# Optimization experiments

Hardware: AMD Instinct MI355X
Metric: run time of the kernel (lower is better)

## Reference

```python
import jax, jax.numpy as jnp
import numpy as np

B, NPG, K, C, IN_DIM, GS_DIM, NBLK, NCLF = 8, 12500, 128, 128, 7, 11, 4, 5
N = B * NPG          # 100000 total nodes
E = N * 8            # 800000 nnz in block-diagonal complex gradient operator


def setup_inputs() -> dict:
    key = jax.random.key(0)
    ks = jax.random.split(key, 20)
    x = jax.random.normal(ks[0], (N, IN_DIM), jnp.float32)
    evals = jax.random.uniform(ks[1], (B, K), jnp.float32) * 10.0  # nonneg eigenvalues
    evecs = jax.random.normal(ks[2], (N, K), jnp.float32) / np.float32(np.sqrt(NPG))
    mass = jax.random.uniform(ks[3], (N,), jnp.float32) + 0.1      # positive lumped mass
    graph_stats = jax.random.normal(ks[4], (B, GS_DIM), jnp.float32)
    batch = jnp.repeat(jnp.arange(B, dtype=jnp.int32), NPG)        # sorted graph ids
    epg = E // B
    offs = jnp.repeat(jnp.arange(B, dtype=jnp.int32) * NPG, epg)   # block-diagonal structure
    grad_rows = jax.random.randint(ks[5], (E,), 0, NPG, jnp.int32) + offs
    grad_cols = jax.random.randint(ks[6], (E,), 0, NPG, jnp.int32) + offs
    grad_vals_re = jax.random.normal(ks[7], (E,), jnp.float32) * 0.1
    grad_vals_im = jax.random.normal(ks[8], (E,), jnp.float32) * 0.1
    grad_n = jnp.full((B,), NPG, jnp.int32)
    s = lambda k, sh, fan: jax.random.normal(k, sh, jnp.float32) / np.float32(np.sqrt(fan))
    W_embed = s(ks[9], (IN_DIM, C), IN_DIM); b_embed = jnp.zeros((C,), jnp.float32)
    t_diff = jax.random.uniform(ks[10], (NBLK, C), jnp.float32) * 0.5 + 1e-3
    A_grad = s(ks[11], (NBLK, C, C), C)
    W1 = s(ks[12], (NBLK, 3 * C, C), 3 * C); b1 = jnp.zeros((NBLK, C), jnp.float32)
    W2 = s(ks[13], (NBLK, C, C), C);         b2 = jnp.zeros((NBLK, C), jnp.float32)
    Wh1 = s(ks[14], (C + GS_DIM, 64), C + GS_DIM); bh1 = jnp.zeros((64,), jnp.float32)
    Wh2 = s(ks[15], (64, NCLF), 64);               bh2 = jnp.zeros((NCLF,), jnp.float32)
    return dict(x=x, evals=evals, evecs=evecs, mass=mass, graph_stats=graph_stats,
                batch=batch, grad_rows=grad_rows, grad_cols=grad_cols,
                grad_vals_re=grad_vals_re, grad_vals_im=grad_vals_im, grad_n=grad_n,
                W_embed=W_embed, b_embed=b_embed, t_diff=t_diff, A_grad=A_grad,
                W1=W1, b1=b1, W2=W2, b2=b2, Wh1=Wh1, bh1=bh1, Wh2=Wh2, bh2=bh2)


def _forward(x, evals, evecs, mass, graph_stats, batch, grad_rows, grad_cols,
             vre, vim, W_embed, b_embed, t_diff, A_grad, W1, b1, W2, b2,
             Wh1, bh1, Wh2, bh2):
    n = x.shape[0]
    ev_r = evecs.reshape(B, NPG, K)              # per-graph spectral basis (equal-size graphs)
    h = jax.nn.relu(x @ W_embed + b_embed)       # embed: [N, C]
    for blk in range(NBLK):                      # fixed small number of blocks
        # --- learned-time spectral diffusion ---
        time = jnp.clip(jnp.abs(t_diff[blk]), 1e-8)            # [C]
        hm = (h * mass[:, None]).reshape(B, NPG, C)
        spec = jnp.einsum('bnk,bnc->bkc', ev_r, hm)            # to_basis: [B, K, C]
        spec = spec * jnp.exp(-evals[:, :, None] * time[None, None, :])
        h_diff = jnp.einsum('bnk,bkc->bnc', ev_r, spec).reshape(n, C)
        # --- block-sparse complex gradient: g = (vre + i*vim) @ h_diff ---
        xg = h_diff[grad_cols]                                 # [E, C] gather
        g_re = jnp.zeros((n, C), h.dtype).at[grad_rows].add(vre[:, None] * xg)
        g_im = jnp.zeros((n, C), h.dtype).at[grad_rows].add(vim[:, None] * xg)
        # --- spatial gradient features: tanh(Re(conj(g) * (A g))) ---
        A = A_grad[blk]
        g_feat = jnp.tanh(g_re * (g_re @ A.T) + g_im * (g_im @ A.T))
        # --- per-vertex MLP + residual (dropout = eval-mode identity) ---
        comb = jnp.concatenate([h, h_diff, g_feat], axis=-1)   # [N, 3C]
        h = h + (jax.nn.relu(comb @ W1[blk] + b1[blk]) @ W2[blk] + b2[blk])
    # --- fuse per-node features with gathered graph stats, node clf head ---
    fused = jnp.concatenate([h, graph_stats[batch]], axis=-1)  # [N, C+11]
    return jax.nn.relu(fused @ Wh1 + bh1) @ Wh2 + bh2          # [N, 5]


def reference(x, evals, evecs, mass, graph_stats, batch, grad_rows, grad_cols,
              grad_vals_re, grad_vals_im, grad_n, W_embed, b_embed, t_diff,
              A_grad, W1, b1, W2, b2, Wh1, bh1, Wh2, bh2):
    # Vectorized replacement of the original per-batch .item() nnz-count loop
    # (histogram of edge rows into per-graph node-offset bins); the block-sparse
    # operator is applied directly with global COO indices so nnz is only a stat.
    node_off = jnp.concatenate([jnp.zeros((1,), jnp.int32),
                                jnp.cumsum(grad_n)[:-1].astype(jnp.int32)])
    _grad_nnz = jnp.bincount(jnp.searchsorted(node_off, grad_rows, side='right') - 1, length=B)
    return _forward(x, evals, evecs, mass, graph_stats, batch, grad_rows, grad_cols,
                    grad_vals_re, grad_vals_im, W_embed, b_embed, t_diff, A_grad,
                    W1, b1, W2, b2, Wh1, bh1, Wh2, bh2)
```

## Files before the change

### kernel.cpp

```cpp
#include <hip/hip_runtime.h>
#include <hip/hip_bf16.h>

#define NNODES 100000
#define NPG    12500
#define NGRAPH 8
#define KD     128
#define CD     128
#define INDIM  7
#define GSDIM  11
#define NBLKS  4
#define NCLF   5
#define NEDGE  800000
#define BCAP   32
#define NPGP   12800
#define TBSPLIT 40
#define TBCHUNK 320
#define NTILES  196
#define NT32    391
#define NT128   98

typedef __attribute__((ext_vector_type(8))) short short8v;
typedef __attribute__((ext_vector_type(4))) float f32x4;
typedef unsigned short u16;
typedef unsigned long long u64;

#define MFMA(acc, a, b) acc = __builtin_amdgcn_mfma_f32_16x16x32_bf16(a, b, acc, 0, 0, 0)

__device__ __forceinline__ u16 f2b(float f) {
  union { __hip_bfloat16 h; u16 u; } cv;
  cv.h = __float2bfloat16(f);
  return cv.u;
}
__device__ __forceinline__ float b2f(u16 u) {
  return __uint_as_float((unsigned)u << 16);
}


__device__ __forceinline__ void stage64_f32(u16* S, const float* src, int ld, int k0, int valid) {
  int t = threadIdx.x, row = t >> 2, kq = t & 3;
  alignas(16) u16 tmp[8] = {0, 0, 0, 0, 0, 0, 0, 0};
  if (row < valid) {
    const float* p = src + (size_t)row * ld + k0 + kq * 8;
    float4 f0 = *(const float4*)p, f1 = *(const float4*)(p + 4);
    tmp[0] = f2b(f0.x); tmp[1] = f2b(f0.y); tmp[2] = f2b(f0.z); tmp[3] = f2b(f0.w);
    tmp[4] = f2b(f1.x); tmp[5] = f2b(f1.y); tmp[6] = f2b(f1.z); tmp[7] = f2b(f1.w);
  }
  *(uint4*)&S[row * 40 + kq * 8] = *(uint4*)tmp;
}

__device__ __forceinline__ void stage64_b16(u16* S, const u16* src, long ld, int k0, int valid) {
  int t = threadIdx.x, row = t >> 2, kq = t & 3;
  uint4 v = make_uint4(0, 0, 0, 0);
  if (row < valid) v = *(const uint4*)(src + (size_t)row * ld + k0 + kq * 8);
  *(uint4*)&S[row * 40 + kq * 8] = v;
}

__device__ __forceinline__ void stage32_b16(u16* S, const u16* src, long ld, int k0, int valid) {
  int t = threadIdx.x;
  if (t < 128) {
    int row = t >> 2, kq = t & 3;
    uint4 v = make_uint4(0, 0, 0, 0);
    if (row < valid) v = *(const uint4*)(src + (size_t)row * ld + k0 + kq * 8);
    *(uint4*)&S[row * 40 + kq * 8] = v;
  }
}

__device__ __forceinline__ void stB512(u16* S, const u16* src, int k0) {
  int t = threadIdx.x, row = t >> 2, kq = t & 3;
  uint4 v = *(const uint4*)(src + (size_t)row * 128 + k0 + kq * 8);
  *(uint4*)&S[row * 40 + kq * 8] = v;
}

__device__ __forceinline__ void stage128_b16(u16* S, const u16* src, long ld, int k0) {
  int t = threadIdx.x, row = t >> 1, half = t & 1;
  const u16* p = src + (size_t)row * ld + k0 + half * 16;
  uint4 v0 = *(const uint4*)p, v1 = *(const uint4*)(p + 8);
  *(uint4*)&S[row * 40 + half * 16] = v0;
  *(uint4*)&S[row * 40 + half * 16 + 8] = v1;
}

__device__ __forceinline__ void stage128_f32(u16* S, const float* src, int ld, int k0) {
  int t = threadIdx.x, row = t >> 1, half = t & 1;
  const float* p = src + (size_t)row * ld + k0 + half * 16;
  float4 f0 = *(const float4*)p, f1 = *(const float4*)(p + 4);
  float4 f2 = *(const float4*)(p + 8), f3 = *(const float4*)(p + 12);
  alignas(16) u16 tmp[16];
  tmp[0] = f2b(f0.x); tmp[1] = f2b(f0.y); tmp[2]  = f2b(f0.z); tmp[3]  = f2b(f0.w);
  tmp[4] = f2b(f1.x); tmp[5] = f2b(f1.y); tmp[6]  = f2b(f1.z); tmp[7]  = f2b(f1.w);
  tmp[8] = f2b(f2.x); tmp[9] = f2b(f2.y); tmp[10] = f2b(f2.z); tmp[11] = f2b(f2.w);
  tmp[12] = f2b(f3.x); tmp[13] = f2b(f3.y); tmp[14] = f2b(f3.z); tmp[15] = f2b(f3.w);
  *(uint4*)&S[row * 40 + half * 16] = *(uint4*)&tmp[0];
  *(uint4*)&S[row * 40 + half * 16 + 8] = *(uint4*)&tmp[8];
}

__device__ __forceinline__ short8v frag(const u16* S, int row0, int l) {
  return *(const short8v*)&S[(row0 + (l & 15)) * 40 + (l >> 4) * 8];
}
__device__ __forceinline__ short8v frag_p(const u16* S, int row0, int l, int pitch, int k0) {
  return *(const short8v*)&S[(row0 + (l & 15)) * pitch + k0 + (l >> 4) * 8];
}


__global__ void k_fill0(float4* p, int n4) {
  int i = blockIdx.x * blockDim.x + threadIdx.x;
  int s = gridDim.x * blockDim.x;
  float4 z = make_float4(0.f, 0.f, 0.f, 0.f);
  for (; i < n4; i += s) p[i] = z;
}

__global__ __launch_bounds__(256) void k_embed2(const float* __restrict__ x,
                                                const float* __restrict__ W,
                                                const float* __restrict__ bv,
                                                const float* __restrict__ mass,
                                                u16* __restrict__ h16,
                                                u16* __restrict__ hmT) {
  int b = blockIdx.x / 200, tile = blockIdx.x % 200;
  int n0 = tile * 64;
  size_t gbase = (size_t)b * NPG;
  int t = threadIdx.x;
  __shared__ float xs[64][8];
  __shared__ float Ws[INDIM][128];
  __shared__ float bs[128];
  __shared__ float ms[64];
  __shared__ float ld[64][132];
  if (t < 128) bs[t] = bv[t];
  for (int i = t; i < INDIM * 128; i += 256) Ws[i >> 7][i & 127] = W[i];
  for (int i = t; i < 64 * INDIM; i += 256) {
    int r = i / INDIM, q = i % INDIM;
    int gn = n0 + r;
    xs[r][q] = (gn < NPG) ? x[(gbase + gn) * INDIM + q] : 0.f;
  }
  if (t < 64) {
    int gn = n0 + t;
    ms[t] = (gn < NPG) ? mass[gbase + gn] : 0.f;
  }
  __syncthreads();
  {
    int row = t & 63, c0 = (t >> 6) * 32;
#pragma unroll
    for (int cc = 0; cc < 32; ++cc) {
      int c = c0 + cc;
      float acc = bs[c];
#pragma unroll
      for (int i = 0; i < INDIM; ++i) acc = fmaf(xs[row][i], Ws[i][c], acc);
      ld[row][c] = fmaxf(acc, 0.f);
    }
  }
  __syncthreads();
  {
    int row = t >> 2, q = t & 3;
    if (n0 + row < NPG) {
      size_t base = (gbase + n0 + row) * (size_t)CD + q * 32;
      alignas(16) u16 tmp[8];
#pragma unroll
      for (int u = 0; u < 4; ++u) {
#pragma unroll
        for (int i = 0; i < 8; ++i) tmp[i] = f2b(ld[row][q * 32 + u * 8 + i]);
        *(uint4*)&h16[base + u * 8] = *(uint4*)tmp;
      }
    }
  }
  {
    int crow = t >> 1, half = t & 1;
    alignas(16) u16 tmp[8];
#pragma unroll
    for (int q = 0; q < 4; ++q) {
      int nb = half * 32 + q * 8;
#pragma unroll
      for (int i = 0; i < 8; ++i) tmp[i] = f2b(ld[nb + i][crow] * ms[nb + i]);
      *(uint4*)&hmT[((size_t)(b * 128 + crow)) * NPGP + n0 + nb] = *(uint4*)tmp;
    }
  }
}

__global__ void k_bucket_place(const int* __restrict__ rows, const int* __restrict__ cols,
                               const float* __restrict__ vre, const float* __restrict__ vim,
                               int* cnt, u64* bucket) {
  int e = blockIdx.x * 256 + threadIdx.x;
  if (e >= NEDGE) return;
  int r = rows[e];
  int pos = atomicAdd(&cnt[r], 1);
  if (pos < BCAP) {
    u64 ent = (u64)(unsigned)cols[e]
            | ((u64)f2b(vre[e]) << 32)
            | ((u64)f2b(vim[e]) << 48);
    bucket[(size_t)r * BCAP + pos] = ent;
  }
}

__global__ void k_gather_ev(const int* __restrict__ cnt, const u64* __restrict__ bucket,
                            const float* __restrict__ evf, const u16* __restrict__ ev16,
                            int useB16,
                            u16* __restrict__ gre, u16* __restrict__ gim) {
  int orig = blockIdx.x;
  int blk  = (orig & 7) * 3125 + (orig >> 3);
  int wv = threadIdx.x >> 6;
  int ln = threadIdx.x & 63;
  int r  = blk * 4 + wv;
  int d = min(cnt[r], BCAP);
  const u64* bk = bucket + (size_t)r * BCAP;
  float2 ra0 = make_float2(0.f, 0.f), ia0 = make_float2(0.f, 0.f);
  float2 ra1 = make_float2(0.f, 0.f), ia1 = make_float2(0.f, 0.f);
  if (useB16) {
    int i = 0;
    for (; i + 2 <= d; i += 2) {
      u64 e0 = bk[i], e1 = bk[i + 1];
      int c0 = (int)(unsigned)e0, c1 = (int)(unsigned)e1;
      float a0 = b2f((u16)(e0 >> 32)), b0 = b2f((u16)(e0 >> 48));
      float a1 = b2f((u16)(e1 >> 32)), b1 = b2f((u16)(e1 >> 48));
      ushort2 u0 = *(const ushort2*)&ev16[(size_t)c0 * KD + ln * 2];
      ushort2 u1 = *(const ushort2*)&ev16[(size_t)c1 * KD + ln * 2];
      float vx0 = b2f(u0.x), vy0 = b2f(u0.y);
      float vx1 = b2f(u1.x), vy1 = b2f(u1.y);
      ra0.x = fmaf(a0, vx0, ra0.x); ra0.y = fmaf(a0, vy0, ra0.y);
      ia0.x = fmaf(b0, vx0, ia0.x); ia0.y = fmaf(b0, vy0, ia0.y);
      ra1.x = fmaf(a1, vx1, ra1.x); ra1.y = fmaf(a1, vy1, ra1.y);
      ia1.x = fmaf(b1, vx1, ia1.x); ia1.y = fmaf(b1, vy1, ia1.y);
    }
    if (i < d) {
      u64 e0 = bk[i];
      int c0 = (int)(unsigned)e0;
      float a0 = b2f((u16)(e0 >> 32)), b0 = b2f((u16)(e0 >> 48));
      ushort2 u0 = *(const ushort2*)&ev16[(size_t)c0 * KD + ln * 2];
      float vx0 = b2f(u0.x), vy0 = b2f(u0.y);
      ra0.x = fmaf(a0, vx0, ra0.x); ra0.y = fmaf(a0, vy0, ra0.y);
      ia0.x = fmaf(b0, vx0, ia0.x); ia0.y = fmaf(b0, vy0, ia0.y);
    }
  } else {
    for (int i = 0; i < d; ++i) {
      u64 e0 = bk[i];
      int c0 = (int)(unsigned)e0;
      float a = b2f((u16)(e0 >> 32)), b = b2f((u16)(e0 >> 48));
      float2 v = *(const float2*)&evf[(size_t)c0 * KD + ln * 2];
      ra0.x = fmaf(a, v.x, ra0.x); ra0.y = fmaf(a, v.y, ra0.y);
      ia0.x = fmaf(b, v.x, ia0.x); ia0.y = fmaf(b, v.y, ia0.y);
    }
  }
  ushort2 ro, io;
  ro.x = f2b(ra0.x + ra1.x); ro.y = f2b(ra0.y + ra1.y);
  io.x = f2b(ia0.x + ia1.x); io.y = f2b(ia0.y + ia1.y);
  *(ushort2*)&gre[(size_t)r * KD + ln * 2] = ro;
  *(ushort2*)&gim[(size_t)r * KD + ln * 2] = io;
}

__global__ void k_prep_w(const float* __restrict__ W1, const float* __restrict__ W2,
                         u16* W1aT, u16* W1bT, u16* W1cT, u16* W2T) {
  int idx = blockIdx.x * 256 + threadIdx.x;
  int blk = idx >> 16, rem = idx & 65535;
  int mat = rem >> 14, e = rem & 16383;
  int j = e >> 7, c = e & 127;
  float v;
  u16* dst;
  if (mat < 3) {
    v = W1[(size_t)blk * 3 * 16384 + (size_t)mat * 16384 + e];
    dst = (mat == 0) ? W1aT : (mat == 1 ? W1bT : W1cT);
  } else {
    v = W2[(size_t)blk * 16384 + e];
    dst = W2T;
  }
  dst[(size_t)blk * 16384 + c * 128 + j] = f2b(v);
}

__global__ void k_prep_head(const float* __restrict__ Wh1, const float* __restrict__ Wh2,
                            u16* __restrict__ B1T, u16* __restrict__ B2T) {
  for (int idx = threadIdx.x; idx < 64 * 160; idx += 256) {
    int c = idx / 160, k = idx % 160;
    B1T[idx] = f2b(k < (CD + GSDIM) ? Wh1[k * 64 + c] : 0.f);
  }
  for (int idx = threadIdx.x; idx < 16 * 64; idx += 256) {
    int c = idx >> 6, k = idx & 63;
    B2T[idx] = f2b(c < NCLF ? Wh2[k * NCLF + c] : 0.f);
  }
}

__global__ void k_transpose_nk(const float* __restrict__ src, u16* __restrict__ dst,
                               u16* __restrict__ ev16, int writeMir) {
  int b = blockIdx.x / 200, tile = blockIdx.x % 200;
  int n0 = tile * 64;
  size_t gbase = (size_t)b * NPG;
  int t = threadIdx.x;
  __shared__ float ld[64][132];
  int row0 = t >> 5, c4 = t & 31;
#pragma unroll
  for (int it = 0; it < 8; ++it) {
    int r = it * 8 + row0;
    int gn = n0 + r;
    float4 v = make_float4(0.f, 0.f, 0.f, 0.f);
    if (gn < NPG) v = *(const float4*)&src[(gbase + gn) * KD + c4 * 4];
    *(float4*)&ld[r][c4 * 4] = v;
    if (writeMir && gn < NPG) {
      ushort4 o;
      o.x = f2b(v.x); o.y = f2b(v.y); o.z = f2b(v.z); o.w = f2b(v.w);
      *(ushort4*)&ev16[(gbase + gn) * KD + c4 * 4] = o;
    }
  }
  __syncthreads();
  int crow = t >> 1, half = t & 1;
  alignas(16) u16 tmp[8];
#pragma unroll
  for (int q = 0; q < 4; ++q) {
    int nb = half * 32 + q * 8;
#pragma unroll
    for (int i = 0; i < 8; ++i) tmp[i] = f2b(ld[nb + i][crow]);
    *(uint4*)&dst[((size_t)(b * 128 + crow)) * NPGP + n0 + nb] = *(uint4*)tmp;
  }
}


__global__ __launch_bounds__(256) void k_tobasis(const u16* __restrict__ evT,
                                                 const u16* __restrict__ hmT,
                                                 float* __restrict__ partials) {
  int g = blockIdx.x;
  int kt = g & 1;
  int s  = (g >> 1) % TBSPLIT;
  int b  = g / (2 * TBSPLIT);
  int t = threadIdx.x, w = t >> 6, l = t & 63;
  __shared__ u16 As[64 * 40];
  __shared__ u16 Bs[128 * 40];
  f32x4 acc[8];
  f32x4 z = {0.f, 0.f, 0.f, 0.f};
#pragma unroll
  for (int j = 0; j < 8; ++j) acc[j] = z;
  const u16* ae = evT + ((size_t)(b * 128 + kt * 64)) * NPGP + s * TBCHUNK;
  const u16* bh = hmT + (size_t)b * 128 * NPGP + s * TBCHUNK;
  for (int ks = 0; ks < TBCHUNK / 32; ++ks) {
    stage64_b16(As, ae, NPGP, ks * 32, 64);
    stage128_b16(Bs, bh, NPGP, ks * 32);
    __syncthreads();
    short8v a = frag(As, w * 16, l);
    __builtin_amdgcn_s_setprio(1);
#pragma unroll
    for (int j = 0; j < 8; ++j) MFMA(acc[j], a, frag(Bs, j * 16, l));
    __builtin_amdgcn_s_setprio(0);
    __syncthreads();
  }
  float* op = partials + (size_t)(b * TBSPLIT + s) * 16384 + kt * 64 * 128;
#pragma unroll
  for (int j = 0; j < 8; ++j)
#pragma unroll
    for (int i = 0; i < 4; ++i) {
      int krow = w * 16 + (l >> 4) * 4 + i;
      int c = j * 16 + (l & 15);
      op[krow * 128 + c] = acc[j][i];
    }
}

__global__ void k_reduce_scale_t(const float* __restrict__ partials,
                                 const float* __restrict__ evals,
                                 const float* __restrict__ td,
                                 float* __restrict__ spec, u16* __restrict__ specT) {
  int b = blockIdx.x >> 6;
  int idx = (blockIdx.x & 63) * 256 + threadIdx.x;
  int k = idx >> 7, c = idx & 127;
  float s = 0.f;
#pragma unroll 8
  for (int sp = 0; sp < TBSPLIT; ++sp)
    s += partials[(size_t)(b * TBSPLIT + sp) * 16384 + idx];
  float tm = fmaxf(fabsf(td[c]), 1e-8f);
  s *= expf(-evals[b * KD + k] * tm);
  spec[(size_t)b * 16384 + idx] = s;
  specT[(size_t)b * 16384 + c * 128 + k] = f2b(s);
}

__global__ __launch_bounds__(256) void k_smallT(const float* __restrict__ Agrad_blk,
                                                const u16* __restrict__ W1bT_blk,
                                                const float* __restrict__ spec,
                                                u16* __restrict__ SAT, u16* __restrict__ M1T) {
  int b = blockIdx.x & 7;
  int job = (blockIdx.x >> 3) & 1;
  int q = blockIdx.x >> 4;
  int t = threadIdx.x, w = t >> 6, l = t & 63;
  __shared__ u16 As[128 * 40];
  __shared__ u16 Bs[128 * 40];
  f32x4 acc[2][2];
  f32x4 z = {0.f, 0.f, 0.f, 0.f};
#pragma unroll
  for (int mi = 0; mi < 2; ++mi) { acc[mi][0] = z; acc[mi][1] = z; }
  for (int ks = 0; ks < 4; ++ks) {
    if (job == 0) stage128_f32(As, Agrad_blk, 128, ks * 32);
    else          stage128_b16(As, W1bT_blk, 128, ks * 32);
    stage128_f32(Bs, spec + (size_t)b * 16384, 128, ks * 32);
    __syncthreads();
    short8v a0 = frag(As, q * 32, l);
    short8v a1 = frag(As, q * 32 + 16, l);
#pragma unroll
    for (int jj = 0; jj < 2; ++jj) {
      short8v bj = frag(Bs, (w * 2 + jj) * 16, l);
      MFMA(acc[0][jj], a0, bj);
      MFMA(acc[1][jj], a1, bj);
    }
    __syncthreads();
  }
  u16* out = (job == 0 ? SAT : M1T) + (size_t)b * 16384;
#pragma unroll
  for (int mi = 0; mi < 2; ++mi)
#pragma unroll
    for (int jj = 0; jj < 2; ++jj)
#pragma unroll
      for (int i = 0; i < 4; ++i)
        out[(q * 32 + mi * 16 + (l >> 4) * 4 + i) * 128 + (w * 2 + jj) * 16 + (l & 15)] =
            f2b(acc[mi][jj][i]);
}

__global__ __launch_bounds__(256) void k_gfeat(const u16* __restrict__ Gre,
                                               const u16* __restrict__ Gim,
                                               const u16* __restrict__ specT,
                                               const u16* __restrict__ SAT,
                                               u16* __restrict__ gf) {
  int b = blockIdx.x / NT32, tile = blockIdx.x % NT32;
  int n0 = tile * 32;
  size_t gbase = (size_t)b * NPG;
  int t = threadIdx.x, w = t >> 6, l = t & 63;
  int r0 = (w & 1) * 16, c0 = (w >> 1) * 64;
  __shared__ u16 Sr[32 * 40];
  __shared__ u16 Si[32 * 40];
  __shared__ u16 Bs[128 * 40];
  __shared__ u16 Ba[128 * 40];
  f32x4 aGR[4], aAR[4], aGI[4], aAI[4];
  f32x4 z = {0.f, 0.f, 0.f, 0.f};
#pragma unroll
  for (int j = 0; j < 4; ++j) { aGR[j] = z; aAR[j] = z; aGI[j] = z; aAI[j] = z; }
  int valid = min(32, NPG - n0);
  const u16* gre = Gre + (gbase + n0) * KD;
  const u16* gim = Gim + (gbase + n0) * KD;
  for (int ks = 0; ks < 4; ++ks) {
    stage32_b16(Sr, gre, KD, ks * 32, valid);
    stage32_b16(Si, gim, KD, ks * 32, valid);
    stage128_b16(Bs, specT + (size_t)b * 16384, 128, ks * 32);
    stage128_b16(Ba, SAT + (size_t)b * 16384, 128, ks * 32);
    __syncthreads();
    short8v fr = frag(Sr, r0, l);
    short8v fi = frag(Si, r0, l);
    __builtin_amdgcn_s_setprio(1);
#pragma unroll
    for (int j = 0; j < 4; ++j) {
      short8v bs = frag(Bs, c0 + j * 16, l);
      short8v ba = frag(Ba, c0 + j * 16, l);
      MFMA(aGR[j], fr, bs);
      MFMA(aAR[j], fr, ba);
      MFMA(aGI[j], fi, bs);
      MFMA(aAI[j], fi, ba);
    }
    __builtin_amdgcn_s_setprio(0);
    __syncthreads();
  }
#pragma unroll
  for (int j = 0; j < 4; ++j) {
    int c = c0 + j * 16 + (l & 15);
#pragma unroll
    for (int i = 0; i < 4; ++i) {
      int n = n0 + r0 + (l >> 4) * 4 + i;
      if (n - n0 < valid) {
        float v = tanhf(fmaf(aGR[j][i], aAR[j][i], aGI[j][i] * aAI[j][i]));
        gf[(gbase + n) * CD + c] = f2b(v);
      }
    }
  }
}

__global__ __launch_bounds__(512) void k_mlp12(const float* __restrict__ evf,
                                               const u16* __restrict__ ev16,
                                               int useB16,
                                               const u16* __restrict__ gf,
                                               const u16* __restrict__ W1aT,
                                               const u16* __restrict__ M1T,
                                               const u16* __restrict__ W1cT,
                                               const float* __restrict__ b1,
                                               const u16* __restrict__ W2T,
                                               const float* __restrict__ b2,
                                               const float* __restrict__ mass,
                                               u16* __restrict__ h16,
                                               u16* __restrict__ hmT,
                                               int writeHmT) {
  int b = blockIdx.x / NT128, tile = blockIdx.x % NT128;
  int n0 = tile * 128;
  size_t gbase = (size_t)b * NPG;
  int t = threadIdx.x, w = t >> 6, l = t & 63;
  __shared__ u16 SH[27136];
  u16* As  = SH;
  u16* Bs  = SH + 5120;
  u16* t1S = SH + 10240;
  u16* Tm  = SH;
  f32x4 acc[8];
  f32x4 z = {0.f, 0.f, 0.f, 0.f};
#pragma unroll
  for (int j = 0; j < 8; ++j) acc[j] = z;
  int valid = min(128, NPG - n0);
  int r0 = w * 16;

  for (int seg = 0; seg < 3; ++seg) {
    const u16* bt = (seg == 0) ? W1aT : (seg == 1 ? M1T + (size_t)b * 16384 : W1cT);
    for (int ks = 0; ks < 4; ++ks) {
      if (seg == 0)      stage64_b16(As, h16 + (gbase + n0) * CD, CD, ks * 32, valid);
      else if (seg == 1) {
        if (useB16) stage64_b16(As, ev16 + (gbase + n0) * KD, KD, ks * 32, valid);
        else        stage64_f32(As, evf + (gbase + n0) * KD, KD, ks * 32, valid);
      }
      else               stage64_b16(As, gf + (gbase + n0) * CD, CD, ks * 32, valid);
      stB512(Bs, bt, ks * 32);
      __syncthreads();
      short8v a = frag(As, r0, l);
      __builtin_amdgcn_s_setprio(1);
#pragma unroll
      for (int j = 0; j < 8; ++j) MFMA(acc[j], a, frag(Bs, j * 16, l));
      __builtin_amdgcn_s_setprio(0);
      __syncthreads();
    }
  }
#pragma unroll
  for (int j = 0; j < 8; ++j) {
    int c = j * 16 + (l & 15);
    float bias = b1[c];
#pragma unroll
    for (int i = 0; i < 4; ++i) {
      int row = r0 + (l >> 4) * 4 + i;
      t1S[row * 132 + c] = f2b(fmaxf(acc[j][i] + bias, 0.f));
    }
  }
  __syncthreads();

#pragma unroll
  for (int j = 0; j < 8; ++j) acc[j] = z;
  for (int ks = 0; ks < 4; ++ks) {
    stB512(Bs, W2T, ks * 32);
    __syncthreads();
    short8v a = frag_p(t1S, r0, l, 132, ks * 32);
    __builtin_amdgcn_s_setprio(1);
#pragma unroll
    for (int j = 0; j < 8; ++j) MFMA(acc[j], a, frag(Bs, j * 16, l));
    __builtin_amdgcn_s_setprio(0);
    __syncthreads();
  }

  float massv[4];
#pragma unroll
  for (int i = 0; i < 4; ++i) {
    int nl = r0 + (l >> 4) * 4 + i;
    massv[i] = (nl < valid) ? mass[gbase + n0 + nl] : 0.f;
  }
#pragma unroll
  for (int j = 0; j < 8; ++j) {
    int c = j * 16 + (l & 15);
    float bias = b2[c];
#pragma unroll
    for (int i = 0; i < 4; ++i) {
      int nl = r0 + (l >> 4) * 4 + i;
      float hv = 0.f;
      if (nl < valid) {
        size_t idx = (gbase + n0 + nl) * (size_t)CD + c;
        hv = b2f(h16[idx]) + acc[j][i] + bias;
        h16[idx] = f2b(hv);
      }
      if (writeHmT) Tm[c * 130 + nl] = f2b(hv * massv[i]);
    }
  }
  if (writeHmT) {
    __syncthreads();
#pragma unroll
    for (int q = 0; q < 4; ++q) {
      int lin = t + q * 512;
      int cc = lin >> 4, chunk = lin & 15;
      *(uint4*)&hmT[((size_t)(b * 128 + cc)) * NPGP + n0 + chunk * 8] =
          *(const uint4*)&Tm[cc * 130 + chunk * 8];
    }
  }
}

__global__ __launch_bounds__(256) void k_head2(
    const u16* __restrict__ h16, const float* __restrict__ gs,
    const int* __restrict__ batch, const u16* __restrict__ B1T,
    const float* __restrict__ bh1, const u16* __restrict__ B2T,
    const float* __restrict__ bh2, float* __restrict__ out) {
  int n0 = blockIdx.x * 64;
  int t = threadIdx.x, w = t >> 6, l = t & 63;
  __shared__ u16 As[64 * 40];
  __shared__ u16 Bs[64 * 40];
  __shared__ u16 zS[64 * 72];
  int valid = min(64, NNODES - n0);
  f32x4 acc1[4];
  f32x4 z = {0.f, 0.f, 0.f, 0.f};
#pragma unroll
  for (int j = 0; j < 4; ++j) acc1[j] = z;
  for (int ks = 0; ks < 5; ++ks) {
    if (ks < 4) {
      stage64_b16(As, h16 + (size_t)n0 * CD, CD, ks * 32, valid);
    } else {
      int row = t >> 2, kq = t & 3;
      alignas(16) u16 tmp[8];
      int bb = (row < valid) ? batch[n0 + row] : 0;
#pragma unroll
      for (int q = 0; q < 8; ++q) {
        int kk = kq * 8 + q;
        float v = (row < valid && kk < GSDIM) ? gs[bb * GSDIM + kk] : 0.f;
        tmp[q] = f2b(v);
      }
      *(uint4*)&As[row * 40 + kq * 8] = *(uint4*)tmp;
    }
    stage64_b16(Bs, B1T, 160, ks * 32, 64);
    __syncthreads();
    short8v a = frag(As, w * 16, l);
#pragma unroll
    for (int j = 0; j < 4; ++j) MFMA(acc1[j], a, frag(Bs, j * 16, l));
    __syncthreads();
  }
#pragma unroll
  for (int j = 0; j < 4; ++j) {
    int c = j * 16 + (l & 15);
    float bias = bh1[c];
#pragma unroll
    for (int i = 0; i < 4; ++i) {
      int row = w * 16 + (l >> 4) * 4 + i;
      zS[row * 72 + c] = f2b(fmaxf(acc1[j][i] + bias, 0.f));
    }
  }
  __syncthreads();
  f32x4 acc2 = z;
  for (int ks = 0; ks < 2; ++ks) {
    stage64_b16(Bs, B2T, 64, ks * 32, 16);
    __syncthreads();
    short8v a2 = frag_p(zS, w * 16, l, 72, ks * 32);
    MFMA(acc2, a2, frag(Bs, 0, l));
    __syncthreads();
  }
  int c = l & 15;
  if (c < NCLF) {
    float bias = bh2[c];
#pragma unroll
    for (int i = 0; i < 4; ++i) {
      int n = n0 + w * 16 + (l >> 4) * 4 + i;
      if (n < NNODES) out[(size_t)n * NCLF + c] = acc2[i] + bias;
    }
  }
}

extern "C" void kernel_launch(void* const* d_in, const int* in_sizes, int n_in,
                              void* d_out, int out_size, void* d_ws, size_t ws_size,
                              hipStream_t stream) {
  const float* x     = (const float*)d_in[0];
  const float* evals = (const float*)d_in[1];
  const float* evecs = (const float*)d_in[2];
  const float* mass  = (const float*)d_in[3];
  const float* gs    = (const float*)d_in[4];
  const int*   batch = (const int*)d_in[5];
  const int*   grows = (const int*)d_in[6];
  const int*   gcols = (const int*)d_in[7];
  const float* vre   = (const float*)d_in[8];
  const float* vim   = (const float*)d_in[9];
  const float* Wemb  = (const float*)d_in[11];
  const float* bemb  = (const float*)d_in[12];
  const float* tdiff = (const float*)d_in[13];
  const float* Agrad = (const float*)d_in[14];
  const float* W1    = (const float*)d_in[15];
  const float* b1    = (const float*)d_in[16];
  const float* W2    = (const float*)d_in[17];
  const float* b2    = (const float*)d_in[18];
  const float* Wh1   = (const float*)d_in[19];
  const float* bh1   = (const float*)d_in[20];
  const float* Wh2   = (const float*)d_in[21];
  const float* bh2   = (const float*)d_in[22];

  char* base = (char*)d_ws;
  size_t off = 0;
  auto alloc = [&](size_t bytes) -> void* {
    void* p = base + off;
    off += (bytes + 255) & ~(size_t)255;
    return p;
  };
  u16*   evT16  = (u16*)alloc((size_t)NGRAPH * 128 * NPGP * 2);
  u16*   hmT    = (u16*)alloc((size_t)NGRAPH * 128 * NPGP * 2);
  u16*   Gre16  = (u16*)alloc((size_t)NNODES * KD * 2);
  u16*   Gim16  = (u16*)alloc((size_t)NNODES * KD * 2);
  u16*   h16    = (u16*)alloc((size_t)NNODES * CD * 2);
  float* spec   = (float*)alloc((size_t)NGRAPH * 16384 * 4);
  u16*   specT16 = (u16*)alloc((size_t)NGRAPH * 16384 * 2);
  u16*   SAT16  = (u16*)alloc((size_t)NGRAPH * 16384 * 2);
  u16*   M1T16  = (u16*)alloc((size_t)NGRAPH * 16384 * 2);
  u16*   W1aT16 = (u16*)alloc((size_t)NBLKS * 16384 * 2);
  u16*   W1bT16 = (u16*)alloc((size_t)NBLKS * 16384 * 2);
  u16*   W1cT16 = (u16*)alloc((size_t)NBLKS * 16384 * 2);
  u16*   W2T16  = (u16*)alloc((size_t)NBLKS * 16384 * 2);
  u16*   B1T16  = (u16*)alloc(64 * 160 * 2);
  u16*   B2T16  = (u16*)alloc(16 * 64 * 2);
  int*   cnt    = (int*)alloc(100352 * 4);
  void*  R      = alloc((size_t)NNODES * BCAP * 8);
  u64*   bucket = (u64*)R;
  float* partials = (float*)R;
  u16*   gf16   = (u16*)R;
  int useEv16 = 0;
  u16* ev16 = nullptr;
  if (off + ((size_t)NNODES * KD * 2 + 256) <= ws_size) {
    ev16 = (u16*)alloc((size_t)NNODES * KD * 2);
    useEv16 = 1;
  }
  float* out    = (float*)d_out;

  k_embed2<<<NGRAPH * 200, 256, 0, stream>>>(x, Wemb, bemb, mass, h16, hmT);
  k_fill0<<<98, 256, 0, stream>>>((float4*)cnt, 100352 / 4);
  k_bucket_place<<<(NEDGE + 255) / 256, 256, 0, stream>>>(grows, gcols, vre, vim,
                                                          cnt, bucket);
  k_transpose_nk<<<NGRAPH * 200, 256, 0, stream>>>(evecs, evT16, ev16, useEv16);
  k_gather_ev<<<NNODES / 4, 256, 0, stream>>>(cnt, bucket, evecs, ev16, useEv16,
                                              Gre16, Gim16);
  k_prep_w<<<1024, 256, 0, stream>>>(W1, W2, W1aT16, W1bT16, W1cT16, W2T16);
  k_prep_head<<<1, 256, 0, stream>>>(Wh1, Wh2, B1T16, B2T16);

  for (int blk = 0; blk < NBLKS; ++blk) {
    k_tobasis<<<NGRAPH * TBSPLIT * 2, 256, 0, stream>>>(evT16, hmT, partials);
    k_reduce_scale_t<<<NGRAPH * 64, 256, 0, stream>>>(partials, evals, tdiff + blk * CD,
                                                      spec, specT16);
    k_smallT<<<64, 256, 0, stream>>>(Agrad + (size_t)blk * 16384,
                                     W1bT16 + (size_t)blk * 16384, spec, SAT16, M1T16);
    k_gfeat<<<NGRAPH * NT32, 256, 0, stream>>>(Gre16, Gim16, specT16, SAT16, gf16);
    k_mlp12<<<NGRAPH * NT128, 512, 0, stream>>>(evecs, ev16, useEv16, gf16,
                                                W1aT16 + (size_t)blk * 16384, M1T16,
                                                W1cT16 + (size_t)blk * 16384,
                                                b1 + blk * CD,
                                                W2T16 + (size_t)blk * 16384,
                                                b2 + blk * CD, mass, h16, hmT,
                                                (blk < NBLKS - 1) ? 1 : 0);
  }
  k_head2<<<(NNODES + 63) / 64, 256, 0, stream>>>(h16, gs, batch, B1T16, bh1,
                                                  B2T16, bh2, out);
}
```

Baseline: 646.4 us.

## Stage full A tile once and double-buffer B in mlp12; split gather rows across waves

In k_mlp12 the whole 128x128 A operand for each segment is now staged into shared memory once, instead of reloading a 32-wide slice every k-step. The B weight slices are prefetched into registers and written into alternating shared buffers, so each k-step needs one barrier instead of two and global loads overlap with MFMA work. k_gather_ev now gives each row to two waves that each handle half of the edges, then combines the halves through shared memory, which doubles the grid and shortens each wave's serial dependency chain. The cost is more shared memory per block (about 55KB), which may reduce occupancy, plus an extra barrier and shared-memory reduction in the gather kernel.

```diff
diff --git a/kernel.cpp b/kernel.cpp
--- a/kernel.cpp
+++ b/kernel.cpp
@@ -15,7 +15,6 @@
 #define NPGP   12800
 #define TBSPLIT 40
 #define TBCHUNK 320
-#define NTILES  196
 #define NT32    391
 #define NT128   98
 
@@ -63,12 +62,6 @@
     if (row < valid) v = *(const uint4*)(src + (size_t)row * ld + k0 + kq * 8);
     *(uint4*)&S[row * 40 + kq * 8] = v;
   }
-}
-
-__device__ __forceinline__ void stB512(u16* S, const u16* src, int k0) {
-  int t = threadIdx.x, row = t >> 2, kq = t & 3;
-  uint4 v = *(const uint4*)(src + (size_t)row * 128 + k0 + kq * 8);
-  *(uint4*)&S[row * 40 + kq * 8] = v;
 }
 
 __device__ __forceinline__ void stage128_b16(u16* S, const u16* src, long ld, int k0) {
@@ -91,6 +84,43 @@
   tmp[12] = f2b(f3.x); tmp[13] = f2b(f3.y); tmp[14] = f2b(f3.z); tmp[15] = f2b(f3.w);
   *(uint4*)&S[row * 40 + half * 16] = *(uint4*)&tmp[0];
   *(uint4*)&S[row * 40 + half * 16 + 8] = *(uint4*)&tmp[8];
+}
+
+__device__ __forceinline__ void stageA_b16(u16* Af, const u16* src, long ld, int valid) {
+  int t = threadIdx.x;
+#pragma unroll
+  for (int q = 0; q < 4; ++q) {
+    int lin = t + q * 512;
+    int row = lin >> 4, kq = lin & 15;
+    uint4 v = make_uint4(0, 0, 0, 0);
+    if (row < valid) v = *(const uint4*)(src + (size_t)row * ld + kq * 8);
+    *(uint4*)&Af[row * 136 + kq * 8] = v;
+  }
+}
+__device__ __forceinline__ void stageA_f32(u16* Af, const float* src, long ld, int valid) {
+  int t = threadIdx.x;
+#pragma unroll
+  for (int q = 0; q < 4; ++q) {
+    int lin = t + q * 512;
+    int row = lin >> 4, kq = lin & 15;
+    alignas(16) u16 tmp[8] = {0, 0, 0, 0, 0, 0, 0, 0};
+    if (row < valid) {
+      const float* p = src + (size_t)row * ld + kq * 8;
+      float4 f0 = *(const float4*)p, f1 = *(const float4*)(p + 4);
+      tmp[0] = f2b(f0.x); tmp[1] = f2b(f0.y); tmp[2] = f2b(f0.z); tmp[3] = f2b(f0.w);
+      tmp[4] = f2b(f1.x); tmp[5] = f2b(f1.y); tmp[6] = f2b(f1.z); tmp[7] = f2b(f1.w);
+    }
+    *(uint4*)&Af[row * 136 + kq * 8] = *(uint4*)tmp;
+  }
+}
+
+__device__ __forceinline__ uint4 ldB(const u16* bt, int k0) {
+  int t = threadIdx.x, row = t >> 2, kq = t & 3;
+  return *(const uint4*)(bt + (size_t)row * 128 + k0 + kq * 8);
+}
+__device__ __forceinline__ void stB(u16* Bs, uint4 v) {
+  int t = threadIdx.x, row = t >> 2, kq = t & 3;
+  *(uint4*)&Bs[row * 40 + kq * 8] = v;
 }
 
 __device__ __forceinline__ short8v frag(const u16* S, int row0, int l) {
@@ -188,59 +218,56 @@
   }
 }
 
-__global__ void k_gather_ev(const int* __restrict__ cnt, const u64* __restrict__ bucket,
-                            const float* __restrict__ evf, const u16* __restrict__ ev16,
-                            int useB16,
-                            u16* __restrict__ gre, u16* __restrict__ gim) {
+__global__ __launch_bounds__(256) void k_gather_ev(
+    const int* __restrict__ cnt, const u64* __restrict__ bucket,
+    const float* __restrict__ evf, const u16* __restrict__ ev16, int useB16,
+    u16* __restrict__ gre, u16* __restrict__ gim) {
   int orig = blockIdx.x;
-  int blk  = (orig & 7) * 3125 + (orig >> 3);
-  int wv = threadIdx.x >> 6;
-  int ln = threadIdx.x & 63;
-  int r  = blk * 4 + wv;
+  int blk  = (orig & 7) * 6250 + (orig >> 3);
+  int t = threadIdx.x;
+  int pair = t >> 7;
+  int wv   = (t >> 6) & 1;
+  int ln   = t & 63;
+  int r = blk * 2 + pair;
   int d = min(cnt[r], BCAP);
   const u64* bk = bucket + (size_t)r * BCAP;
-  float2 ra0 = make_float2(0.f, 0.f), ia0 = make_float2(0.f, 0.f);
-  float2 ra1 = make_float2(0.f, 0.f), ia1 = make_float2(0.f, 0.f);
+  int i0 = wv ? (d >> 1) : 0;
+  int i1 = wv ? d : (d >> 1);
+  float2 ra = make_float2(0.f, 0.f), ia = make_float2(0.f, 0.f);
   if (useB16) {
-    int i = 0;
-    for (; i + 2 <= d; i += 2) {
-      u64 e0 = bk[i], e1 = bk[i + 1];
-      int c0 = (int)(unsigned)e0, c1 = (int)(unsigned)e1;
-      float a0 = b2f((u16)(e0 >> 32)), b0 = b2f((u16)(e0 >> 48));
-      float a1 = b2f((u16)(e1 >> 32)), b1 = b2f((u16)(e1 >> 48));
-      ushort2 u0 = *(const ushort2*)&ev16[(size_t)c0 * KD + ln * 2];
-      ushort2 u1 = *(const ushort2*)&ev16[(size_t)c1 * KD + ln * 2];
-      float vx0 = b2f(u0.x), vy0 = b2f(u0.y);
-      float vx1 = b2f(u1.x), vy1 = b2f(u1.y);
-      ra0.x = fmaf(a0, vx0, ra0.x); ra0.y = fmaf(a0, vy0, ra0.y);
-      ia0.x = fmaf(b0, vx0, ia0.x); ia0.y = fmaf(b0, vy0, ia0.y);
-      ra1.x = fmaf(a1, vx1, ra1.x); ra1.y = fmaf(a1, vy1, ra1.y);
-      ia1.x = fmaf(b1, vx1, ia1.x); ia1.y = fmaf(b1, vy1, ia1.y);
-    }
-    if (i < d) {
+    for (int i = i0; i < i1; ++i) {
       u64 e0 = bk[i];
       int c0 = (int)(unsigned)e0;
-      float a0 = b2f((u16)(e0 >> 32)), b0 = b2f((u16)(e0 >> 48));
+      float a = b2f((u16)(e0 >> 32)), b = b2f((u16)(e0 >> 48));
       ushort2 u0 = *(const ushort2*)&ev16[(size_t)c0 * KD + ln * 2];
-      float vx0 = b2f(u0.x), vy0 = b2f(u0.y);
-      ra0.x = fmaf(a0, vx0, ra0.x); ra0.y = fmaf(a0, vy0, ra0.y);
-      ia0.x = fmaf(b0, vx0, ia0.x); ia0.y = fmaf(b0, vy0, ia0.y);
+      ra.x = fmaf(a, b2f(u0.x), ra.x); ra.y = fmaf(a, b2f(u0.y), ra.y);
+      ia.x = fmaf(b, b2f(u0.x), ia.x); ia.y = fmaf(b, b2f(u0.y), ia.y);
     }
   } else {
-    for (int i = 0; i < d; ++i) {
+    for (int i = i0; i < i1; ++i) {
       u64 e0 = bk[i];
       int c0 = (int)(unsigned)e0;
       float a = b2f((u16)(e0 >> 32)), b = b2f((u16)(e0 >> 48));
       float2 v = *(const float2*)&evf[(size_t)c0 * KD + ln * 2];
-      ra0.x = fmaf(a, v.x, ra0.x); ra0.y = fmaf(a, v.y, ra0.y);
-      ia0.x = fmaf(b, v.x, ia0.x); ia0.y = fmaf(b, v.y, ia0.y);
-    }
-  }
-  ushort2 ro, io;
-  ro.x = f2b(ra0.x + ra1.x); ro.y = f2b(ra0.y + ra1.y);
-  io.x = f2b(ia0.x + ia1.x); io.y = f2b(ia0.y + ia1.y);
-  *(ushort2*)&gre[(size_t)r * KD + ln * 2] = ro;
-  *(ushort2*)&gim[(size_t)r * KD + ln * 2] = io;
+      ra.x = fmaf(a, v.x, ra.x); ra.y = fmaf(a, v.y, ra.y);
+      ia.x = fmaf(b, v.x, ia.x); ia.y = fmaf(b, v.y, ia.y);
+    }
+  }
+  __shared__ float part[2][64][4];
+  if (wv == 1) {
+    part[pair][ln][0] = ra.x; part[pair][ln][1] = ra.y;
+    part[pair][ln][2] = ia.x; part[pair][ln][3] = ia.y;
+  }
+  __syncthreads();
+  if (wv == 0) {
+    ra.x += part[pair][ln][0]; ra.y += part[pair][ln][1];
+    ia.x += part[pair][ln][2]; ia.y += part[pair][ln][3];
+    ushort2 ro, io;
+    ro.x = f2b(ra.x); ro.y = f2b(ra.y);
+    io.x = f2b(ia.x); io.y = f2b(ia.y);
+    *(ushort2*)&gre[(size_t)r * KD + ln * 2] = ro;
+    *(ushort2*)&gim[(size_t)r * KD + ln * 2] = io;
+  }
 }
 
 __global__ void k_prep_w(const float* __restrict__ W1, const float* __restrict__ W2,
@@ -476,11 +503,12 @@
   int n0 = tile * 128;
   size_t gbase = (size_t)b * NPG;
   int t = threadIdx.x, w = t >> 6, l = t & 63;
-  __shared__ u16 SH[27136];
-  u16* As  = SH;
-  u16* Bs  = SH + 5120;
-  u16* t1S = SH + 10240;
+  __shared__ u16 SH[27648];
+  u16* Af  = SH;
+  u16* t1S = SH;
   u16* Tm  = SH;
+  u16* Bs0 = SH + 17408;
+  u16* Bs1 = SH + 22528;
   f32x4 acc[8];
   f32x4 z = {0.f, 0.f, 0.f, 0.f};
 #pragma unroll
@@ -490,20 +518,25 @@
 
   for (int seg = 0; seg < 3; ++seg) {
     const u16* bt = (seg == 0) ? W1aT : (seg == 1 ? M1T + (size_t)b * 16384 : W1cT);
+    if (seg == 0)      stageA_b16(Af, h16 + (gbase + n0) * CD, CD, valid);
+    else if (seg == 1) {
+      if (useB16) stageA_b16(Af, ev16 + (gbase + n0) * KD, KD, valid);
+      else        stageA_f32(Af, evf + (gbase + n0) * KD, KD, valid);
+    }
+    else               stageA_b16(Af, gf + (gbase + n0) * CD, CD, valid);
+    stB(Bs0, ldB(bt, 0));
+    __syncthreads();
+#pragma unroll
     for (int ks = 0; ks < 4; ++ks) {
-      if (seg == 0)      stage64_b16(As, h16 + (gbase + n0) * CD, CD, ks * 32, valid);
-      else if (seg == 1) {
-        if (useB16) stage64_b16(As, ev16 + (gbase + n0) * KD, KD, ks * 32, valid);
-        else        stage64_f32(As, evf + (gbase + n0) * KD, KD, ks * 32, valid);
-      }
-      else               stage64_b16(As, gf + (gbase + n0) * CD, CD, ks * 32, valid);
-      stB512(Bs, bt, ks * 32);
-      __syncthreads();
-      short8v a = frag(As, r0, l);
+      uint4 bvn;
+      if (ks < 3) bvn = ldB(bt, (ks + 1) * 32);
+      short8v a = frag_p(Af, r0, l, 136, ks * 32);
+      u16* Bcur = (ks & 1) ? Bs1 : Bs0;
       __builtin_amdgcn_s_setprio(1);
 #pragma unroll
-      for (int j = 0; j < 8; ++j) MFMA(acc[j], a, frag(Bs, j * 16, l));
+      for (int j = 0; j < 8; ++j) MFMA(acc[j], a, frag(Bcur, j * 16, l));
       __builtin_amdgcn_s_setprio(0);
+      if (ks < 3) stB((ks & 1) ? Bs0 : Bs1, bvn);
       __syncthreads();
     }
   }
@@ -517,18 +550,22 @@
       t1S[row * 132 + c] = f2b(fmaxf(acc[j][i] + bias, 0.f));
     }
   }
+  stB(Bs0, ldB(W2T, 0));
   __syncthreads();
 
 #pragma unroll
   for (int j = 0; j < 8; ++j) acc[j] = z;
+#pragma unroll
   for (int ks = 0; ks < 4; ++ks) {
-    stB512(Bs, W2T, ks * 32);
-    __syncthreads();
+    uint4 bvn;
+    if (ks < 3) bvn = ldB(W2T, (ks + 1) * 32);
     short8v a = frag_p(t1S, r0, l, 132, ks * 32);
+    u16* Bcur = (ks & 1) ? Bs1 : Bs0;
     __builtin_amdgcn_s_setprio(1);
 #pragma unroll
-    for (int j = 0; j < 8; ++j) MFMA(acc[j], a, frag(Bs, j * 16, l));
+    for (int j = 0; j < 8; ++j) MFMA(acc[j], a, frag(Bcur, j * 16, l));
     __builtin_amdgcn_s_setprio(0);
+    if (ks < 3) stB((ks & 1) ? Bs0 : Bs1, bvn);
     __syncthreads();
   }
 
@@ -699,7 +736,7 @@
   k_bucket_place<<<(NEDGE + 255) / 256, 256, 0, stream>>>(grows, gcols, vre, vim,
                                                           cnt, bucket);
   k_transpose_nk<<<NGRAPH * 200, 256, 0, stream>>>(evecs, evT16, ev16, useEv16);
-  k_gather_ev<<<NNODES / 4, 256, 0, stream>>>(cnt, bucket, evecs, ev16, useEv16,
+  k_gather_ev<<<NNODES / 2, 256, 0, stream>>>(cnt, bucket, evecs, ev16, useEv16,
                                               Gre16, Gim16);
   k_prep_w<<<1024, 256, 0, stream>>>(W1, W2, W1aT16, W1bT16, W1cT16, W2T16);
   k_prep_head<<<1, 256, 0, stream>>>(Wh1, Wh2, B1T16, B2T16);
```

Measured after the change: 683.3 us. 1.06x slower.
